# Optimization experiments

Measured on AMD Instinct MI355X. Metric: run time of the kernel, lower is better.

## Reference

```python
import jax, jax.numpy as jnp
import numpy as np


def setup_inputs() -> dict:
    key = jax.random.key(0)
    k1, k2 = jax.random.split(key)
    tensor_1 = jax.random.normal(k1, (8192, 256), dtype=jnp.float32)
    tensor_2 = jax.random.normal(k2, (16384, 256), dtype=jnp.float32)
    return {"tensor_1": tensor_1, "tensor_2": tensor_2}


def reference(tensor_1, tensor_2):
    # L2-normalize along the feature dim (matches torch .norm(dim=-1), no eps)
    n1 = tensor_1 / jnp.linalg.norm(tensor_1, axis=-1, keepdims=True)  # [N, d]
    n2 = tensor_2 / jnp.linalg.norm(tensor_2, axis=-1, keepdims=True)  # [M, d]
    cos_sim = jnp.einsum("nd,md->nm", n1, n2)  # [N, M] cosine similarity
    top3, _ = jax.lax.top_k(cos_sim, 3)        # [N, 3]
    return top3.mean(axis=-1)                  # [N]
```

## Files before the change

### kernel.cpp

```cpp
#include <hip/hip_runtime.h>
#include <hip/hip_bf16.h>
#include <stdint.h>

#define N1 8192
#define N2 16384
#define DIM 256
#define NSPLIT 16
#define BM 128
#define BN 128
#define BK 128
#define COLS_PER_SPLIT (N2 / NSPLIT)
#define NT_PER_SPLIT (COLS_PER_SPLIT / BN)
#define NPART (NSPLIT * 2)

typedef short v8s  __attribute__((ext_vector_type(8)));
typedef float f32x4 __attribute__((ext_vector_type(4)));

#define GLD16(g, l)                                                                         \
  __builtin_amdgcn_global_load_lds((const __attribute__((address_space(1))) uint32_t*)(g),  \
                                   (__attribute__((address_space(3))) uint32_t*)(l), 16, 0, 0)

__device__ __forceinline__ void top3_insert(float v, float& t0, float& t1, float& t2) {
    float nt1 = __builtin_amdgcn_fmed3f(v, t0, t1);
    float nt2 = __builtin_amdgcn_fmed3f(v, t1, t2);
    t0 = fmaxf(t0, v);
    t1 = nt1;
    t2 = nt2;
}

__global__ __launch_bounds__(256) void normalize_kernel(
        const float* __restrict__ inA, const float* __restrict__ inB,
        __hip_bfloat16* __restrict__ outA, __hip_bfloat16* __restrict__ outB) {
    const int gw   = blockIdx.x * 4 + (threadIdx.x >> 6);
    const int lane = threadIdx.x & 63;
    const float* in;
    __hip_bfloat16* out;
    int row;
    if (gw < N1) { in = inA; out = outA; row = gw; }
    else         { in = inB; out = outB; row = gw - N1; }
    const float4 v = *(const float4*)(in + (size_t)row * DIM + lane * 4);
    float s = v.x * v.x + v.y * v.y + v.z * v.z + v.w * v.w;
    #pragma unroll
    for (int off = 32; off; off >>= 1) s += __shfl_xor(s, off, 64);
    const float inv = 1.0f / sqrtf(s);
    __hip_bfloat16 o[4];
    o[0] = __float2bfloat16(v.x * inv);
    o[1] = __float2bfloat16(v.y * inv);
    o[2] = __float2bfloat16(v.z * inv);
    o[3] = __float2bfloat16(v.w * inv);
    *(uint2*)(out + (size_t)row * DIM + lane * 4) = *(uint2*)o;
}

__global__ __launch_bounds__(256, 2) void gemm_top3_kernel(
        const __hip_bfloat16* __restrict__ A, const __hip_bfloat16* __restrict__ B,
        float* __restrict__ partial) {
    __shared__ char smem[32768 + 32768];
    char* tileA = smem;
    char* tileB = smem + 32768;

    const int tid  = threadIdx.x;
    const int wave = tid >> 6;
    const int lane = tid & 63;
    const int lo   = lane & 15;
    const int quad = lane >> 4;
    const int rb    = blockIdx.x >> 4;
    const int split = blockIdx.x & 15;
    const int row0 = rb * BM;
    const int C0   = split * COLS_PER_SPLIT;
    const int wr = (wave >> 1) * 64;
    const int wc = (wave & 1) * 64;

    const int lr  = lane >> 4;
    const int s16 = lane & 15;

    const char* Agbase = (const char*)A + ((size_t)(row0 + wave * 32 + lr)) * 512;
    const char* Bgbase = (const char*)B + ((size_t)(C0   + wave * 32 + lr)) * 512;
    char* AldsBase = tileA + wave * 32 * 256;
    char* BldsBase = tileB + wave * 32 * 256;

    int aoff[4], boff[4];
    #pragma unroll
    for (int ks = 0; ks < 4; ks++) {
        const int swz = ((ks * 4 + quad) ^ lo) * 16;
        aoff[ks] = (wr + lo) * 256 + swz;
        boff[ks] = (wc + lo) * 256 + swz;
    }

    float t0[16], t1[16], t2[16];
    #pragma unroll
    for (int i = 0; i < 16; i++) { t0[i] = -1e30f; t1[i] = -1e30f; t2[i] = -1e30f; }

    for (int nt = 0; nt < NT_PER_SPLIT; ++nt) {
        f32x4 acc[4][4];
        #pragma unroll
        for (int kk = 0; kk < 2; kk++) {
            __syncthreads();
            #pragma unroll
            for (int j = 0; j < 8; j++) {
                const int sxj = (s16 ^ ((j * 4 + lr) & 15)) * 16;
                GLD16(Agbase + (size_t)j * 2048 + kk * 256 + sxj, AldsBase + j * 1024);
                GLD16(Bgbase + (size_t)nt * 65536 + (size_t)j * 2048 + kk * 256 + sxj,
                      BldsBase + j * 1024);
            }
            __syncthreads();
            #pragma unroll
            for (int ks = 0; ks < 4; ks++) {
                v8s af[4];
                #pragma unroll
                for (int rt = 0; rt < 4; rt++)
                    af[rt] = *(const v8s*)(tileA + aoff[ks] + rt * 4096);
                #pragma unroll
                for (int ct = 0; ct < 4; ct++) {
                    v8s bf = *(const v8s*)(tileB + boff[ks] + ct * 4096);
                    #pragma unroll
                    for (int rt = 0; rt < 4; rt++) {
                        if (kk == 0 && ks == 0)
                            acc[rt][ct] = __builtin_amdgcn_mfma_f32_16x16x32_bf16(
                                af[rt], bf, (f32x4){0.f, 0.f, 0.f, 0.f}, 0, 0, 0);
                        else
                            acc[rt][ct] = __builtin_amdgcn_mfma_f32_16x16x32_bf16(
                                af[rt], bf, acc[rt][ct], 0, 0, 0);
                    }
                }
            }
        }
        #pragma unroll
        for (int rt = 0; rt < 4; rt++)
            #pragma unroll
            for (int r = 0; r < 4; r++) {
                const int i = rt * 4 + r;
                #pragma unroll
                for (int ct = 0; ct < 4; ct++)
                    top3_insert(acc[rt][ct][r], t0[i], t1[i], t2[i]);
            }
    }

    #pragma unroll
    for (int step = 1; step < 16; step <<= 1) {
        #pragma unroll
        for (int i = 0; i < 16; i++) {
            float b0 = __shfl_xor(t0[i], step, 64);
            float b1 = __shfl_xor(t1[i], step, 64);
            float b2 = __shfl_xor(t2[i], step, 64);
            top3_insert(b0, t0[i], t1[i], t2[i]);
            top3_insert(b1, t0[i], t1[i], t2[i]);
            top3_insert(b2, t0[i], t1[i], t2[i]);
        }
    }

    if (lo == 0) {
        #pragma unroll
        for (int rt = 0; rt < 4; rt++)
            #pragma unroll
            for (int r = 0; r < 4; r++) {
                const int i = rt * 4 + r;
                const int row = row0 + wr + rt * 16 + quad * 4 + r;
                float* p = partial + ((size_t)row * NPART + (split * 2 + (wave & 1))) * 3;
                p[0] = t0[i]; p[1] = t1[i]; p[2] = t2[i];
            }
    }
}

__global__ __launch_bounds__(256) void merge_kernel(
        const float* __restrict__ partial, float* __restrict__ out) {
    const int row = blockIdx.x * 256 + threadIdx.x;
    if (row >= N1) return;
    const float* p = partial + (size_t)row * NPART * 3;
    float t0 = -1e30f, t1 = -1e30f, t2 = -1e30f;
    #pragma unroll
    for (int i = 0; i < NPART * 3; i++) top3_insert(p[i], t0, t1, t2);
    out[row] = (t0 + t1 + t2) * (1.0f / 3.0f);
}

extern "C" void kernel_launch(void* const* d_in, const int* in_sizes, int n_in,
                              void* d_out, int out_size, void* d_ws, size_t ws_size,
                              hipStream_t stream) {
    const float* tA = (const float*)d_in[0];
    const float* tB = (const float*)d_in[1];
    float* out = (float*)d_out;

    __hip_bfloat16* An = (__hip_bfloat16*)d_ws;
    __hip_bfloat16* Bn = An + (size_t)N1 * DIM;
    float* partial = (float*)(Bn + (size_t)N2 * DIM);

    normalize_kernel<<<(N1 + N2) / 4, 256, 0, stream>>>(tA, tB, An, Bn);
    gemm_top3_kernel<<<(N1 / BM) * NSPLIT, 256, 0, stream>>>(An, Bn, partial);
    merge_kernel<<<N1 / 256, 256, 0, stream>>>(partial, out);
}
```

Before: 153.9 us.

## Restructure GEMM into 128x256 output tiles with one column tile per block

The GEMM now gives each block a single 128x256 output tile over 64x64 blocks, instead of looping over column tiles within a split. It stages K in 64-element chunks with a new swizzle and raises MFMA priority with s_setprio. It then reduces top-3 across waves in shared memory before writing 64 partials per row. The normalize kernel processes four rows per wave and the merge kernel splits each row across four lanes with float4 loads. The intent is more parallelism and better load balance, at the cost of more partials to merge and more accumulator registers.

```diff
diff --git a/kernel.cpp b/kernel.cpp
--- a/kernel.cpp
+++ b/kernel.cpp
@@ -5,13 +5,11 @@
 #define N1 8192
 #define N2 16384
 #define DIM 256
-#define NSPLIT 16
 #define BM 128
-#define BN 128
-#define BK 128
-#define COLS_PER_SPLIT (N2 / NSPLIT)
-#define NT_PER_SPLIT (COLS_PER_SPLIT / BN)
-#define NPART (NSPLIT * 2)
+#define BN 256
+#define RB 64
+#define CB 64
+#define NPART CB
 
 typedef short v8s  __attribute__((ext_vector_type(8)));
 typedef float f32x4 __attribute__((ext_vector_type(4)));
@@ -31,145 +29,170 @@
 __global__ __launch_bounds__(256) void normalize_kernel(
         const float* __restrict__ inA, const float* __restrict__ inB,
         __hip_bfloat16* __restrict__ outA, __hip_bfloat16* __restrict__ outB) {
-    const int gw   = blockIdx.x * 4 + (threadIdx.x >> 6);
+    const int wave = threadIdx.x >> 6;
     const int lane = threadIdx.x & 63;
+    const int rgrp = lane >> 4;
+    const int li   = lane & 15;
+    const int gr   = blockIdx.x * 16 + wave * 4 + rgrp;
     const float* in;
     __hip_bfloat16* out;
     int row;
-    if (gw < N1) { in = inA; out = outA; row = gw; }
-    else         { in = inB; out = outB; row = gw - N1; }
-    const float4 v = *(const float4*)(in + (size_t)row * DIM + lane * 4);
-    float s = v.x * v.x + v.y * v.y + v.z * v.z + v.w * v.w;
-    #pragma unroll
-    for (int off = 32; off; off >>= 1) s += __shfl_xor(s, off, 64);
+    if (gr < N1) { in = inA; out = outA; row = gr; }
+    else         { in = inB; out = outB; row = gr - N1; }
+    const float* rp = in + (size_t)row * DIM + li * 4;
+    float4 v[4];
+    #pragma unroll
+    for (int j = 0; j < 4; ++j) v[j] = *(const float4*)(rp + j * 64);
+    float s = 0.f;
+    #pragma unroll
+    for (int j = 0; j < 4; ++j)
+        s += v[j].x * v[j].x + v[j].y * v[j].y + v[j].z * v[j].z + v[j].w * v[j].w;
+    #pragma unroll
+    for (int off = 8; off; off >>= 1) s += __shfl_xor(s, off, 64);
     const float inv = 1.0f / sqrtf(s);
-    __hip_bfloat16 o[4];
-    o[0] = __float2bfloat16(v.x * inv);
-    o[1] = __float2bfloat16(v.y * inv);
-    o[2] = __float2bfloat16(v.z * inv);
-    o[3] = __float2bfloat16(v.w * inv);
-    *(uint2*)(out + (size_t)row * DIM + lane * 4) = *(uint2*)o;
+    __hip_bfloat16* wp = out + (size_t)row * DIM + li * 4;
+    #pragma unroll
+    for (int j = 0; j < 4; ++j) {
+        __hip_bfloat16 o[4];
+        o[0] = __float2bfloat16(v[j].x * inv);
+        o[1] = __float2bfloat16(v[j].y * inv);
+        o[2] = __float2bfloat16(v[j].z * inv);
+        o[3] = __float2bfloat16(v[j].w * inv);
+        *(uint2*)(wp + j * 64) = *(uint2*)o;
+    }
 }
 
 __global__ __launch_bounds__(256, 2) void gemm_top3_kernel(
         const __hip_bfloat16* __restrict__ A, const __hip_bfloat16* __restrict__ B,
         float* __restrict__ partial) {
-    __shared__ char smem[32768 + 32768];
-    char* tileA = smem;
-    char* tileB = smem + 32768;
+    __shared__ char smem[49152];
 
     const int tid  = threadIdx.x;
     const int wave = tid >> 6;
     const int lane = tid & 63;
     const int lo   = lane & 15;
     const int quad = lane >> 4;
-    const int rb    = blockIdx.x >> 4;
-    const int split = blockIdx.x & 15;
+    const int wm   = wave >> 1;
+    const int wn   = wave & 1;
+    const int rb   = blockIdx.x & 63;
+    const int cb   = blockIdx.x >> 6;
     const int row0 = rb * BM;
-    const int C0   = split * COLS_PER_SPLIT;
-    const int wr = (wave >> 1) * 64;
-    const int wc = (wave & 1) * 64;
-
-    const int lr  = lane >> 4;
-    const int s16 = lane & 15;
-
-    const char* Agbase = (const char*)A + ((size_t)(row0 + wave * 32 + lr)) * 512;
-    const char* Bgbase = (const char*)B + ((size_t)(C0   + wave * 32 + lr)) * 512;
-    char* AldsBase = tileA + wave * 32 * 256;
-    char* BldsBase = tileB + wave * 32 * 256;
-
-    int aoff[4], boff[4];
-    #pragma unroll
-    for (int ks = 0; ks < 4; ks++) {
-        const int swz = ((ks * 4 + quad) ^ lo) * 16;
-        aoff[ks] = (wr + lo) * 256 + swz;
-        boff[ks] = (wc + lo) * 256 + swz;
-    }
-
-    float t0[16], t1[16], t2[16];
-    #pragma unroll
-    for (int i = 0; i < 16; i++) { t0[i] = -1e30f; t1[i] = -1e30f; t2[i] = -1e30f; }
-
-    for (int nt = 0; nt < NT_PER_SPLIT; ++nt) {
-        f32x4 acc[4][4];
-        #pragma unroll
-        for (int kk = 0; kk < 2; kk++) {
-            __syncthreads();
-            #pragma unroll
-            for (int j = 0; j < 8; j++) {
-                const int sxj = (s16 ^ ((j * 4 + lr) & 15)) * 16;
-                GLD16(Agbase + (size_t)j * 2048 + kk * 256 + sxj, AldsBase + j * 1024);
-                GLD16(Bgbase + (size_t)nt * 65536 + (size_t)j * 2048 + kk * 256 + sxj,
-                      BldsBase + j * 1024);
-            }
-            __syncthreads();
-            #pragma unroll
-            for (int ks = 0; ks < 4; ks++) {
-                v8s af[4];
+    const int col0 = cb * BN;
+
+    const int srow8 = lane >> 3;
+    const int sslot = lane & 7;
+    const size_t goff = (size_t)(wave * 8 + srow8) * 512 + (size_t)((sslot ^ srow8) << 4);
+    const char* Ag = (const char*)A + (size_t)row0 * 512 + goff;
+    const char* Bg = (const char*)B + (size_t)col0 * 512 + goff;
+    char* tileA = smem;
+    char* tileB = smem + 16384;
+
+    int aoff[2], boff[2];
+    #pragma unroll
+    for (int ks = 0; ks < 2; ++ks) {
+        const int swz = (((ks * 4 + quad) ^ (lo & 7)) << 4);
+        aoff[ks] = (wm * 64 + lo) * 128 + swz;
+        boff[ks] = 16384 + (wn * 128 + lo) * 128 + swz;
+    }
+
+    f32x4 acc[4][8];
+
+    #pragma unroll
+    for (int kt = 0; kt < 4; ++kt) {
+        __syncthreads();
+        #pragma unroll
+        for (int g = 0; g < 4; ++g)
+            GLD16(Ag + (size_t)g * 16384 + kt * 128, tileA + g * 4096 + wave * 1024);
+        #pragma unroll
+        for (int g = 0; g < 8; ++g)
+            GLD16(Bg + (size_t)g * 16384 + kt * 128, tileB + g * 4096 + wave * 1024);
+        __syncthreads();
+        #pragma unroll
+        for (int ks = 0; ks < 2; ++ks) {
+            v8s af[4];
+            #pragma unroll
+            for (int rt = 0; rt < 4; ++rt)
+                af[rt] = *(const v8s*)(smem + aoff[ks] + rt * 2048);
+            __builtin_amdgcn_s_setprio(1);
+            #pragma unroll
+            for (int ct = 0; ct < 8; ++ct) {
+                v8s bf = *(const v8s*)(smem + boff[ks] + ct * 2048);
                 #pragma unroll
-                for (int rt = 0; rt < 4; rt++)
-                    af[rt] = *(const v8s*)(tileA + aoff[ks] + rt * 4096);
-                #pragma unroll
-                for (int ct = 0; ct < 4; ct++) {
-                    v8s bf = *(const v8s*)(tileB + boff[ks] + ct * 4096);
-                    #pragma unroll
-                    for (int rt = 0; rt < 4; rt++) {
-                        if (kk == 0 && ks == 0)
-                            acc[rt][ct] = __builtin_amdgcn_mfma_f32_16x16x32_bf16(
-                                af[rt], bf, (f32x4){0.f, 0.f, 0.f, 0.f}, 0, 0, 0);
-                        else
-                            acc[rt][ct] = __builtin_amdgcn_mfma_f32_16x16x32_bf16(
-                                af[rt], bf, acc[rt][ct], 0, 0, 0);
-                    }
+                for (int rt = 0; rt < 4; ++rt) {
+                    if (kt == 0 && ks == 0)
+                        acc[rt][ct] = __builtin_amdgcn_mfma_f32_16x16x32_bf16(
+                            af[rt], bf, (f32x4){0.f, 0.f, 0.f, 0.f}, 0, 0, 0);
+                    else
+                        acc[rt][ct] = __builtin_amdgcn_mfma_f32_16x16x32_bf16(
+                            af[rt], bf, acc[rt][ct], 0, 0, 0);
                 }
             }
+            __builtin_amdgcn_s_setprio(0);
         }
-        #pragma unroll
-        for (int rt = 0; rt < 4; rt++)
-            #pragma unroll
-            for (int r = 0; r < 4; r++) {
-                const int i = rt * 4 + r;
-                #pragma unroll
-                for (int ct = 0; ct < 4; ct++)
-                    top3_insert(acc[rt][ct][r], t0[i], t1[i], t2[i]);
+    }
+
+    __syncthreads();
+    float* fbuf = (float*)smem;
+    #pragma unroll
+    for (int rt = 0; rt < 4; ++rt) {
+        #pragma unroll
+        for (int r = 0; r < 4; ++r) {
+            float u0 = -1e30f, u1 = -1e30f, u2 = -1e30f;
+            #pragma unroll
+            for (int ct = 0; ct < 8; ++ct)
+                top3_insert(acc[rt][ct][r], u0, u1, u2);
+            #pragma unroll
+            for (int step = 1; step < 16; step <<= 1) {
+                float b0 = __shfl_xor(u0, step, 64);
+                float b1 = __shfl_xor(u1, step, 64);
+                float b2 = __shfl_xor(u2, step, 64);
+                top3_insert(b0, u0, u1, u2);
+                top3_insert(b1, u0, u1, u2);
+                top3_insert(b2, u0, u1, u2);
             }
-    }
-
-    #pragma unroll
-    for (int step = 1; step < 16; step <<= 1) {
-        #pragma unroll
-        for (int i = 0; i < 16; i++) {
-            float b0 = __shfl_xor(t0[i], step, 64);
-            float b1 = __shfl_xor(t1[i], step, 64);
-            float b2 = __shfl_xor(t2[i], step, 64);
-            top3_insert(b0, t0[i], t1[i], t2[i]);
-            top3_insert(b1, t0[i], t1[i], t2[i]);
-            top3_insert(b2, t0[i], t1[i], t2[i]);
+            if (lo == 0) {
+                const int row = wm * 64 + rt * 16 + quad * 4 + r;
+                float* p = fbuf + (row * 2 + wn) * 3;
+                p[0] = u0; p[1] = u1; p[2] = u2;
+            }
         }
     }
-
-    if (lo == 0) {
-        #pragma unroll
-        for (int rt = 0; rt < 4; rt++)
-            #pragma unroll
-            for (int r = 0; r < 4; r++) {
-                const int i = rt * 4 + r;
-                const int row = row0 + wr + rt * 16 + quad * 4 + r;
-                float* p = partial + ((size_t)row * NPART + (split * 2 + (wave & 1))) * 3;
-                p[0] = t0[i]; p[1] = t1[i]; p[2] = t2[i];
-            }
+    __syncthreads();
+    if (tid < BM) {
+        const float* p = fbuf + tid * 6;
+        float u0 = p[0], u1 = p[1], u2 = p[2];
+        top3_insert(p[3], u0, u1, u2);
+        top3_insert(p[4], u0, u1, u2);
+        top3_insert(p[5], u0, u1, u2);
+        float* o = partial + ((size_t)(row0 + tid) * NPART + cb) * 3;
+        o[0] = u0; o[1] = u1; o[2] = u2;
     }
 }
 
 __global__ __launch_bounds__(256) void merge_kernel(
         const float* __restrict__ partial, float* __restrict__ out) {
-    const int row = blockIdx.x * 256 + threadIdx.x;
-    if (row >= N1) return;
-    const float* p = partial + (size_t)row * NPART * 3;
+    const int row = blockIdx.x * 64 + (threadIdx.x >> 2);
+    const int sub = threadIdx.x & 3;
+    const float4* p = (const float4*)(partial + (size_t)row * NPART * 3) + sub * 12;
     float t0 = -1e30f, t1 = -1e30f, t2 = -1e30f;
     #pragma unroll
-    for (int i = 0; i < NPART * 3; i++) top3_insert(p[i], t0, t1, t2);
-    out[row] = (t0 + t1 + t2) * (1.0f / 3.0f);
+    for (int i = 0; i < 12; ++i) {
+        float4 v = p[i];
+        top3_insert(v.x, t0, t1, t2);
+        top3_insert(v.y, t0, t1, t2);
+        top3_insert(v.z, t0, t1, t2);
+        top3_insert(v.w, t0, t1, t2);
+    }
+    #pragma unroll
+    for (int step = 1; step < 4; step <<= 1) {
+        float b0 = __shfl_xor(t0, step, 64);
+        float b1 = __shfl_xor(t1, step, 64);
+        float b2 = __shfl_xor(t2, step, 64);
+        top3_insert(b0, t0, t1, t2);
+        top3_insert(b1, t0, t1, t2);
+        top3_insert(b2, t0, t1, t2);
+    }
+    if (sub == 0) out[row] = (t0 + t1 + t2) * (1.0f / 3.0f);
 }
 
 extern "C" void kernel_launch(void* const* d_in, const int* in_sizes, int n_in,
@@ -183,7 +206,7 @@
     __hip_bfloat16* Bn = An + (size_t)N1 * DIM;
     float* partial = (float*)(Bn + (size_t)N2 * DIM);
 
-    normalize_kernel<<<(N1 + N2) / 4, 256, 0, stream>>>(tA, tB, An, Bn);
-    gemm_top3_kernel<<<(N1 / BM) * NSPLIT, 256, 0, stream>>>(An, Bn, partial);
-    merge_kernel<<<N1 / 256, 256, 0, stream>>>(partial, out);
-}
+    normalize_kernel<<<(N1 + N2) / 16, 256, 0, stream>>>(tA, tB, An, Bn);
+    gemm_top3_kernel<<<RB * CB, 256, 0, stream>>>(An, Bn, partial);
+    merge_kernel<<<N1 / 64, 256, 0, stream>>>(partial, out);
+}
```

Result: slower. 179.1 us (+16.4%).
